# Optimization experiments

Measured on AMD Instinct MI355X. Metric: run time of the kernel, lower is better.

## Reference

```python
import jax, jax.numpy as jnp
import numpy as np

B, Q, C, N_PER, GS = 8, 2048, 256, 64, 8
H1, H2 = 256, 64
EPS = 1e-5


def make_grid():
    a = jnp.linspace(-0.1, 0.1, GS)
    gx, gy = jnp.meshgrid(a, a, indexing='ij')  # torch.meshgrid default 'ij'
    return jnp.stack([gx.reshape(-1), gy.reshape(-1)], axis=1)  # (n, 2)


def setup_inputs() -> dict:
    key = jax.random.key(0)
    ks = jax.random.split(key, 10)
    s = lambda k, shp, fan: jax.random.normal(k, shp, jnp.float32) / np.sqrt(fan)
    return {
        'tokens': jax.random.normal(ks[0], (B, Q, C), jnp.float32),
        'grid': make_grid(),
        'Wc': s(ks[1], (C, 3), C), 'bc': jnp.zeros((3,), jnp.float32),
        'W1': s(ks[2], (C + 2, H1), C + 2), 'b1': jnp.zeros((H1,), jnp.float32),
        'gamma1': jnp.ones((H1,), jnp.float32), 'beta1': jnp.zeros((H1,), jnp.float32),
        'W2': s(ks[3], (H1, H2), H1), 'b2': jnp.zeros((H2,), jnp.float32),
        'gamma2': jnp.ones((H2,), jnp.float32), 'beta2': jnp.zeros((H2,), jnp.float32),
        'W3': s(ks[4], (H2, 3), H2), 'b3': jnp.zeros((3,), jnp.float32),
    }


def batchnorm(x, gamma, beta):
    # BatchNorm1d in training mode: stats over batch (B*Q) and length (n) dims,
    # per channel (last axis here).
    mean = jnp.mean(x, axis=(0, 1, 2), keepdims=True)
    var = jnp.var(x, axis=(0, 1, 2), keepdims=True)
    return gamma * (x - mean) * jax.lax.rsqrt(var + EPS) + beta


def reference(tokens, grid, Wc, bc, W1, b1, gamma1, beta1, W2, b2, gamma2, beta2, W3, b3):
    coarse = tokens @ Wc + bc  # (B, Q, 3)
    # conv1 (1x1) on concat([tokens_expanded, grid]) == split matmul + broadcast add;
    # avoids materializing the (B,Q,n,C+2) concat explicitly.
    tok_part = tokens @ W1[:C]                 # (B, Q, H1)
    grid_part = grid @ W1[C:]                  # (n, H1)
    h = tok_part[:, :, None, :] + grid_part[None, None, :, :] + b1  # (B, Q, n, H1)
    h = jax.nn.relu(batchnorm(h, gamma1, beta1))
    h = jnp.einsum('bqnc,cd->bqnd', h, W2) + b2  # (B, Q, n, H2)
    h = jax.nn.relu(batchnorm(h, gamma2, beta2))
    disp = jnp.einsum('bqnc,cd->bqnd', h, W3) + b3  # (B, Q, n, 3)
    fine = (coarse[:, :, None, :] + disp).reshape(B, Q * N_PER, 3)
    return coarse, fine
```

## Files before the change

### kernel.cpp

```cpp
#include <hip/hip_runtime.h>
#include <hip/hip_bf16.h>

#define ROWS 16384
#define C_   256
#define H1_  256
#define H2_  64
#define EPSN 1e-5f

typedef __bf16 bf16x8 __attribute__((ext_vector_type(8)));
typedef __bf16 bf16x4 __attribute__((ext_vector_type(4)));
typedef __bf16 bf16x2 __attribute__((ext_vector_type(2)));
typedef float  f32x4  __attribute__((ext_vector_type(4)));
typedef float  f32x2  __attribute__((ext_vector_type(2)));

__device__ __forceinline__ bf16x2 cvt2(float a, float b) {
#if __has_builtin(__builtin_amdgcn_cvt_pk_bf16_f32)
    return __builtin_bit_cast(bf16x2, __builtin_amdgcn_cvt_pk_bf16_f32(a, b));
#else
    bf16x2 r; r[0] = (__bf16)a; r[1] = (__bf16)b; return r;
#endif
}

__device__ __forceinline__ void barrier_lgkm() {
    asm volatile("s_waitcnt lgkmcnt(0)" ::: "memory");
    __builtin_amdgcn_sched_barrier(0);
    __builtin_amdgcn_s_barrier();
    __builtin_amdgcn_sched_barrier(0);
}

__global__ __launch_bounds__(256) void k0_pack(const float* __restrict__ W1,
                                               const float* __restrict__ W2,
                                               const float* __restrict__ W3,
                                               __bf16* __restrict__ W1p,
                                               __bf16* __restrict__ W2p,
                                               __bf16* __restrict__ W3p,
                                               float* __restrict__ zero_base) {
    int idx = blockIdx.x * 256 + threadIdx.x;
    if (idx < 65536) {
        int j = idx & 7, l = (idx >> 3) & 63, rest = idx >> 9;
        int ks = rest & 7, CT = rest >> 3;
        int k = ks * 32 + ((l >> 4) << 3) + j;
        int c = CT * 16 + (l & 15);
        W1p[idx] = (__bf16)W1[k * H1_ + c];
    } else {
        int i2 = idx - 65536;
        int j = i2 & 7, l = (i2 >> 3) & 63, rest = i2 >> 9;
        int ks = rest & 7, CK = rest >> 3;
        int k = ks * 32 + ((l >> 4) << 3) + j;
        int c2 = CK * 16 + (l & 15);
        W2p[i2] = (__bf16)W2[k * H2_ + c2];
    }
    if (idx < 1024) {
        int j = idx & 7, l = (idx >> 3) & 63, ks = idx >> 9;
        int k = ks * 32 + ((l >> 4) << 3) + j;
        int c = l & 15;
        W3p[idx] = (c < 3) ? (__bf16)W3[k * 3 + c] : (__bf16)0.f;
    }
    if (idx < 24576) zero_base[idx] = 0.0f;
}

__device__ __forceinline__ void prep_ctx(const float* __restrict__ grid,
                                         const float* __restrict__ W1,
                                         const float* __restrict__ a1p, int c0,
                                         f32x2* wgx2, f32x2* wgy2, float* A_) {
#pragma unroll
    for (int j = 0; j < 8; ++j) A_[j] = grid[2 * j + 1];
    f32x4 a0 = *(const f32x4*)(a1p + c0), a1h = *(const f32x4*)(a1p + c0 + 4);
    f32x4 x0 = *(const f32x4*)(W1 + C_ * H1_ + c0), x1 = *(const f32x4*)(W1 + C_ * H1_ + c0 + 4);
    f32x4 y0 = *(const f32x4*)(W1 + (C_ + 1) * H1_ + c0), yh = *(const f32x4*)(W1 + (C_ + 1) * H1_ + c0 + 4);
    float av[8] = {a0[0], a0[1], a0[2], a0[3], a1h[0], a1h[1], a1h[2], a1h[3]};
    float wx[8] = {x0[0], x0[1], x0[2], x0[3], x1[0], x1[1], x1[2], x1[3]};
    float wy[8] = {y0[0], y0[1], y0[2], y0[3], yh[0], yh[1], yh[2], yh[3]};
#pragma unroll
    for (int e = 0; e < 4; ++e) {
        wgx2[e][0] = av[2 * e] * wx[2 * e];     wgx2[e][1] = av[2 * e + 1] * wx[2 * e + 1];
        wgy2[e][0] = av[2 * e] * wy[2 * e];     wgy2[e][1] = av[2 * e + 1] * wy[2 * e + 1];
    }
}

__device__ __forceinline__ void stage16(__bf16* __restrict__ y1, int w, int c0, int nh,
                                        const float* __restrict__ a1p,
                                        const float* __restrict__ d1p,
                                        const f32x2* wgx2, const f32x2* wgy2,
                                        const float* A_, f32x4 t0, f32x4 t1) {
    f32x4 a0 = *(const f32x4*)(a1p + c0), a1h = *(const f32x4*)(a1p + c0 + 4);
    f32x4 d0 = *(const f32x4*)(d1p + c0), d1h = *(const f32x4*)(d1p + c0 + 4);
    int chunk = c0 >> 3;
    f32x2 base2[4];
    base2[0][0] = fmaf(a0[0], t0[0], d0[0]);  base2[0][1] = fmaf(a0[1], t0[1], d0[1]);
    base2[1][0] = fmaf(a0[2], t0[2], d0[2]);  base2[1][1] = fmaf(a0[3], t0[3], d0[3]);
    base2[2][0] = fmaf(a1h[0], t1[0], d1h[0]); base2[2][1] = fmaf(a1h[1], t1[1], d1h[1]);
    base2[3][0] = fmaf(a1h[2], t1[2], d1h[2]); base2[3][1] = fmaf(a1h[3], t1[3], d1h[3]);
#pragma unroll
    for (int ih = 0; ih < 2; ++ih) {
        float axs = A_[2 * w + ih];
        f32x2 ax2 = {axs, axs};
        f32x2 tc2[4];
#pragma unroll
        for (int e = 0; e < 4; ++e) tc2[e] = __builtin_elementwise_fma(wgx2[e], ax2, base2[e]);
#pragma unroll
        for (int kk = 0; kk < 4; ++kk) {
            int iy = nh + 2 * kk;
            float ays = A_[iy];
            f32x2 ay2 = {ays, ays};
            f32x2 z = {0.f, 0.f};
            int n = w * 16 + ih * 8 + iy;
            bf16x8 out;
            bf16x2* o2 = (bf16x2*)&out;
#pragma unroll
            for (int e = 0; e < 4; ++e) {
                f32x2 v = __builtin_elementwise_max(
                    __builtin_elementwise_fma(wgy2[e], ay2, tc2[e]), z);
                o2[e] = cvt2(v[0], v[1]);
            }
            *(bf16x8*)(&y1[n * 256 + ((chunk ^ iy) << 3)]) = out;
        }
    }
}

__global__ __launch_bounds__(256) void k1a(const float* __restrict__ tokens,
                                           const __bf16* __restrict__ W1p,
                                           const float* __restrict__ Wc,
                                           const float* __restrict__ bc,
                                           float* __restrict__ tokpart,
                                           float* __restrict__ coarse,
                                           float* __restrict__ p1s,
                                           float* __restrict__ p1q) {
    __shared__ __align__(16) __bf16 Al[16 * 264];
    int t = threadIdx.x, w = t >> 6, l = t & 63;
    int quad = l >> 4, col = l & 15;
    int rowbase = (blockIdx.x >> 1) * 16;
    int colhalf = blockIdx.x & 1;
    int slot = blockIdx.x & 31;

    bf16x8 bfr[16];
#pragma unroll
    for (int ctl = 0; ctl < 2; ++ctl)
#pragma unroll
        for (int ks = 0; ks < 8; ++ks) {
            int CT = colhalf * 8 + w * 2 + ctl;
            bfr[ctl * 8 + ks] = *(const bf16x8*)(W1p + (((CT * 8 + ks) * 64 + l) * 8));
        }
    {
        int r = t >> 4, cb = (t & 15) * 16;
        const float* src = tokens + (size_t)(rowbase + r) * C_ + cb;
        f32x4 t0 = *(const f32x4*)(src);
        f32x4 t1 = *(const f32x4*)(src + 4);
        f32x4 t2 = *(const f32x4*)(src + 8);
        f32x4 t3 = *(const f32x4*)(src + 12);
        bf16x8 v0, v1;
        bf16x2* p0 = (bf16x2*)&v0; bf16x2* p1 = (bf16x2*)&v1;
        p0[0] = cvt2(t0[0], t0[1]); p0[1] = cvt2(t0[2], t0[3]);
        p0[2] = cvt2(t1[0], t1[1]); p0[3] = cvt2(t1[2], t1[3]);
        p1[0] = cvt2(t2[0], t2[1]); p1[1] = cvt2(t2[2], t2[3]);
        p1[2] = cvt2(t3[0], t3[1]); p1[3] = cvt2(t3[2], t3[3]);
        *(bf16x8*)(&Al[r * 264 + cb]) = v0;
        *(bf16x8*)(&Al[r * 264 + cb + 8]) = v1;
    }
    barrier_lgkm();

    bf16x8 af[8];
#pragma unroll
    for (int ks = 0; ks < 8; ++ks)
        af[ks] = *(const bf16x8*)(&Al[col * 264 + ks * 32 + quad * 8]);

#pragma unroll
    for (int ctl = 0; ctl < 2; ++ctl) {
        f32x4 acc = {0.f, 0.f, 0.f, 0.f};
#pragma unroll
        for (int ks = 0; ks < 8; ++ks)
            acc = __builtin_amdgcn_mfma_f32_16x16x32_bf16(af[ks], bfr[ctl * 8 + ks], acc, 0, 0, 0);
        int c = colhalf * 128 + w * 32 + ctl * 16 + col;
        float s = 0.f, q = 0.f;
#pragma unroll
        for (int rr = 0; rr < 4; ++rr) {
            float v = acc[rr];
            tokpart[(size_t)(rowbase + quad * 4 + rr) * C_ + c] = v;
            s += v; q += v * v;
        }
        s += __shfl_xor(s, 16, 64); s += __shfl_xor(s, 32, 64);
        q += __shfl_xor(q, 16, 64); q += __shfl_xor(q, 32, 64);
        if (l < 16) {
            int cc = colhalf * 128 + w * 32 + ctl * 16 + l;
            atomicAdd(p1s + slot * C_ + cc, s);
            atomicAdd(p1q + slot * C_ + cc, q);
        }
    }
    if (colhalf == 0) {
        const f32x4* wcp = (const f32x4*)(Wc + l * 12);
        f32x4 wa = wcp[0], wb = wcp[1], wv = wcp[2];
        float wcl[12] = {wa[0], wa[1], wa[2], wa[3], wb[0], wb[1], wb[2], wb[3],
                         wv[0], wv[1], wv[2], wv[3]};
#pragma unroll
        for (int rr = 0; rr < 4; ++rr) {
            int r = w * 4 + rr;
            bf16x4 tv4 = *(const bf16x4*)(&Al[r * 264 + l * 4]);
            float p[3] = {0.f, 0.f, 0.f};
#pragma unroll
            for (int i = 0; i < 4; ++i) {
                float tvf = (float)tv4[i];
#pragma unroll
                for (int j = 0; j < 3; ++j) p[j] = fmaf(tvf, wcl[i * 3 + j], p[j]);
            }
#pragma unroll
            for (int off = 1; off < 64; off <<= 1)
#pragma unroll
                for (int j = 0; j < 3; ++j) p[j] += __shfl_xor(p[j], off, 64);
            if (l == 0) {
#pragma unroll
                for (int j = 0; j < 3; ++j)
                    coarse[(size_t)(rowbase + r) * 3 + j] = p[j] + bc[j];
            }
        }
    }
}

__global__ void k1b(const float* __restrict__ grid, const float* __restrict__ W1,
                    const float* __restrict__ gamma1, const float* __restrict__ beta1,
                    const float* __restrict__ p1s, const float* __restrict__ p1q,
                    float* __restrict__ a1o, float* __restrict__ d1o) {
    int t = threadIdx.x;
    float S = 0.f, Qq = 0.f;
    for (int s = 0; s < 32; ++s) { S += p1s[s * C_ + t]; Qq += p1q[s * C_ + t]; }
    float mean_t = S / (float)ROWS;
    float var_t = Qq / (float)ROWS - mean_t * mean_t;
    float wx = W1[C_ * H1_ + t];
    float wy = W1[(C_ + 1) * H1_ + t];
    float mg = 0.f, qg = 0.f;
    for (int n = 0; n < 64; ++n) {
        float gv = grid[2 * n] * wx + grid[2 * n + 1] * wy;
        mg += gv; qg += gv * gv;
    }
    mg *= (1.f / 64.f);
    float var_g = qg * (1.f / 64.f) - mg * mg;
    float a1 = gamma1[t] * rsqrtf(var_t + var_g + EPSN);
    a1o[t] = a1;
    d1o[t] = beta1[t] - a1 * (mean_t + mg);
}

template <bool SPILL>
__global__ __launch_bounds__(256) void k2(const float* __restrict__ tokpart,
                                          const float* __restrict__ grid,
                                          const float* __restrict__ W1,
                                          const __bf16* __restrict__ W2p,
                                          const float* __restrict__ a1,
                                          const float* __restrict__ d1,
                                          float* __restrict__ p2s,
                                          float* __restrict__ p2q,
                                          __bf16* __restrict__ h2s) {
    __shared__ __align__(16) __bf16 y1[64 * 256];
    int t = threadIdx.x, w = t >> 6, l = t & 63;
    int quad = l >> 4, col = l & 15;
    int wn = w >> 1, wc = w & 1;
    int c0 = (l & 31) * 8, nh = l >> 5;
    int sw = col & 7;

    bf16x8 bfr[16];
#pragma unroll
    for (int ck = 0; ck < 2; ++ck)
#pragma unroll
        for (int ks = 0; ks < 8; ++ks)
            bfr[ck * 8 + ks] = *(const bf16x8*)(W2p + ((((wc * 2 + ck) * 8 + ks) * 64 + l) * 8));

    f32x2 wgx2[4], wgy2[4]; float A_[8];
    prep_ctx(grid, W1, a1, c0, wgx2, wgy2, A_);

    float s[2][4] = {}, q[2][4] = {};

    const float* tokbase = tokpart + (size_t)blockIdx.x * 8 * C_;
    f32x4 t0 = *(const f32x4*)(tokbase + c0);
    f32x4 t1 = *(const f32x4*)(tokbase + c0 + 4);

#pragma unroll 1
    for (int r8 = 0; r8 < 8; ++r8) {
        int row = blockIdx.x * 8 + r8;
        int nr = (r8 < 7) ? (r8 + 1) : 7;
        f32x4 n0 = *(const f32x4*)(tokbase + (size_t)nr * C_ + c0);
        f32x4 n1 = *(const f32x4*)(tokbase + (size_t)nr * C_ + c0 + 4);

        stage16(y1, w, c0, nh, a1, d1, wgx2, wgy2, A_, t0, t1);
        barrier_lgkm();
#pragma unroll
        for (int rt = 0; rt < 2; ++rt) {
            int rowb = (wn * 32 + rt * 16 + col) * 256;
            bf16x8 af[8];
#pragma unroll
            for (int ks = 0; ks < 8; ++ks)
                af[ks] = *(const bf16x8*)(&y1[rowb + (((ks * 4 + quad) ^ sw) << 3)]);
#pragma unroll
            for (int ck = 0; ck < 2; ++ck) {
                f32x4 acc = {0.f, 0.f, 0.f, 0.f};
#pragma unroll
                for (int ks = 0; ks < 8; ++ks)
                    acc = __builtin_amdgcn_mfma_f32_16x16x32_bf16(bfr[ck * 8 + ks], af[ks], acc, 0, 0, 0);
#pragma unroll
                for (int rr = 0; rr < 4; ++rr) {
                    s[ck][rr] += acc[rr];
                    q[ck][rr] += acc[rr] * acc[rr];
                }
                if constexpr (SPILL) {
                    bf16x4 v; bf16x2* v2 = (bf16x2*)&v;
                    v2[0] = cvt2(acc[0], acc[1]);
                    v2[1] = cvt2(acc[2], acc[3]);
                    *(bf16x4*)(h2s + (size_t)row * 4096 +
                               ((wn * 2 + rt) * 4 + wc * 2 + ck) * 256 + l * 4) = v;
                }
            }
        }
        barrier_lgkm();
        t0 = n0; t1 = n1;
    }
    int slot = ((blockIdx.x << 1) | wn) & 63;
#pragma unroll
    for (int ck = 0; ck < 2; ++ck)
#pragma unroll
        for (int rr = 0; rr < 4; ++rr) {
            float sv = s[ck][rr], qv = q[ck][rr];
            sv += __shfl_xor(sv, 1, 64); sv += __shfl_xor(sv, 2, 64);
            sv += __shfl_xor(sv, 4, 64); sv += __shfl_xor(sv, 8, 64);
            qv += __shfl_xor(qv, 1, 64); qv += __shfl_xor(qv, 2, 64);
            qv += __shfl_xor(qv, 4, 64); qv += __shfl_xor(qv, 8, 64);
            if (col == 0) {
                int c2 = wc * 32 + ck * 16 + quad * 4 + rr;
                atomicAdd(p2s + slot * H2_ + c2, sv);
                atomicAdd(p2q + slot * H2_ + c2, qv);
            }
        }
}

__global__ void k2b(const float* __restrict__ p2s, const float* __restrict__ p2q,
                    const float* __restrict__ gamma2, const float* __restrict__ beta2,
                    float* __restrict__ a2o, float* __restrict__ d2o) {
    int t = threadIdx.x;
    float S = 0.f, Qq = 0.f;
    for (int s = 0; s < 64; ++s) { S += p2s[s * H2_ + t]; Qq += p2q[s * H2_ + t]; }
    const float invN = 1.f / ((float)ROWS * 64.f);
    float mean = S * invN;
    float var = Qq * invN - mean * mean;
    float a2 = gamma2[t] * rsqrtf(var + EPSN);
    a2o[t] = a2;
    d2o[t] = beta2[t] - a2 * mean;
}

__global__ __launch_bounds__(256) void k3s(const __bf16* __restrict__ h2s,
                                           const float* __restrict__ a2,
                                           const float* __restrict__ d2p,
                                           const __bf16* __restrict__ W3p,
                                           const float* __restrict__ b3,
                                           const float* __restrict__ coarse,
                                           float* __restrict__ fine) {
    __shared__ __align__(16) __bf16 y2l[4][16 * 64];
    __shared__ __align__(16) float finebuf[8 * 192];
    int t = threadIdx.x, w = t >> 6, l = t & 63;
    int quad = l >> 4, col = l & 15;
    int sw = col & 7;

    bf16x8 wfr[2];
#pragma unroll
    for (int ks = 0; ks < 2; ++ks)
        wfr[ks] = *(const bf16x8*)(W3p + ((ks * 64 + l) * 8));

    float a2v[16], d2v[16];
#pragma unroll
    for (int ck = 0; ck < 4; ++ck)
#pragma unroll
        for (int rr = 0; rr < 4; ++rr) {
            int c2 = ck * 16 + quad * 4 + rr;
            a2v[ck * 4 + rr] = a2[c2];
            d2v[ck * 4 + rr] = d2p[c2];
        }
    float b3v = (col < 3) ? b3[col] : 0.f;
    __bf16* yw = &y2l[w][0];

#pragma unroll 1
    for (int r8 = 0; r8 < 8; ++r8) {
        int row = blockIdx.x * 8 + r8;
        const __bf16* src = h2s + (size_t)row * 4096 + l * 4;
        bf16x4 u[4];
#pragma unroll
        for (int ck = 0; ck < 4; ++ck)
            u[ck] = *(const bf16x4*)(src + (w * 4 + ck) * 256);
#pragma unroll
        for (int ck = 0; ck < 4; ++ck) {
            float y0 = fmaxf(fmaf(a2v[ck * 4 + 0], (float)u[ck][0], d2v[ck * 4 + 0]), 0.f);
            float y1v = fmaxf(fmaf(a2v[ck * 4 + 1], (float)u[ck][1], d2v[ck * 4 + 1]), 0.f);
            float y2 = fmaxf(fmaf(a2v[ck * 4 + 2], (float)u[ck][2], d2v[ck * 4 + 2]), 0.f);
            float y3 = fmaxf(fmaf(a2v[ck * 4 + 3], (float)u[ck][3], d2v[ck * 4 + 3]), 0.f);
            bf16x4 v; bf16x2* v2 = (bf16x2*)&v;
            v2[0] = cvt2(y0, y1v); v2[1] = cvt2(y2, y3);
            int chunk = ck * 2 + (quad >> 1);
            *(bf16x4*)(&yw[col * 64 + ((chunk ^ sw) << 3) + (quad & 1) * 4]) = v;
        }
        bf16x8 af2[2];
#pragma unroll
        for (int ks = 0; ks < 2; ++ks)
            af2[ks] = *(const bf16x8*)(&yw[col * 64 + (((ks * 4 + quad) ^ sw) << 3)]);
        f32x4 acc = {0.f, 0.f, 0.f, 0.f};
        acc = __builtin_amdgcn_mfma_f32_16x16x32_bf16(af2[0], wfr[0], acc, 0, 0, 0);
        acc = __builtin_amdgcn_mfma_f32_16x16x32_bf16(af2[1], wfr[1], acc, 0, 0, 0);
        if (col < 3) {
            float cj = coarse[row * 3 + col] + b3v;
#pragma unroll
            for (int rr = 0; rr < 4; ++rr)
                finebuf[r8 * 192 + (w * 16 + quad * 4 + rr) * 3 + col] = acc[rr] + cj;
        }
    }
    __syncthreads();
    {
        float* dst = fine + (size_t)blockIdx.x * 1536;
        const f32x4* fb = (const f32x4*)finebuf;
        *(f32x4*)(dst + 4 * t) = fb[t];
        if (t < 128) *(f32x4*)(dst + 1024 + 4 * t) = fb[256 + t];
    }
}

__global__ __launch_bounds__(256) void k3r(const float* __restrict__ tokpart,
                                           const float* __restrict__ grid,
                                           const float* __restrict__ W1,
                                           const __bf16* __restrict__ W2p,
                                           const float* __restrict__ a1,
                                           const float* __restrict__ d1,
                                           const __bf16* __restrict__ W3p,
                                           const float* __restrict__ a2,
                                           const float* __restrict__ d2p,
                                           const float* __restrict__ b3,
                                           const float* __restrict__ coarse,
                                           float* __restrict__ fine) {
    __shared__ __align__(16) __bf16 y1[64 * 256];
    __shared__ __align__(16) __bf16 y2l[64 * 72];
    __shared__ __align__(16) float finebuf[8 * 192];
    int t = threadIdx.x, w = t >> 6, l = t & 63;
    int quad = l >> 4, col = l & 15;
    int wn = w >> 1, wc = w & 1;
    int c0 = (l & 31) * 8, nh = l >> 5;
    int sw = col & 7;

    bf16x8 bfr[16];
#pragma unroll
    for (int ck = 0; ck < 2; ++ck)
#pragma unroll
        for (int ks = 0; ks < 8; ++ks)
            bfr[ck * 8 + ks] = *(const bf16x8*)(W2p + ((((wc * 2 + ck) * 8 + ks) * 64 + l) * 8));
    bf16x8 wfr[2];
#pragma unroll
    for (int ks = 0; ks < 2; ++ks)
        wfr[ks] = *(const bf16x8*)(W3p + ((ks * 64 + l) * 8));

    f32x2 wgx2[4], wgy2[4]; float A_[8];
    prep_ctx(grid, W1, a1, c0, wgx2, wgy2, A_);

    float a2v[8], d2v[8];
#pragma unroll
    for (int ck = 0; ck < 2; ++ck)
#pragma unroll
        for (int rr = 0; rr < 4; ++rr) {
            int c2 = wc * 32 + ck * 16 + quad * 4 + rr;
            a2v[ck * 4 + rr] = a2[c2];
            d2v[ck * 4 + rr] = d2p[c2];
        }
    float b3v = (col < 3) ? b3[col] : 0.f;

#pragma unroll 1
    for (int r8 = 0; r8 < 8; ++r8) {
        int row = blockIdx.x * 8 + r8;
        const float* tokrow = tokpart + (size_t)row * C_;
        f32x4 t0 = *(const f32x4*)(tokrow + c0);
        f32x4 t1 = *(const f32x4*)(tokrow + c0 + 4);
        stage16(y1, w, c0, nh, a1, d1, wgx2, wgy2, A_, t0, t1);
        __syncthreads();
#pragma unroll
        for (int rt = 0; rt < 2; ++rt) {
            int rowb = (wn * 32 + rt * 16 + col) * 256;
            bf16x8 af[8];
#pragma unroll
            for (int ks = 0; ks < 8; ++ks)
                af[ks] = *(const bf16x8*)(&y1[rowb + (((ks * 4 + quad) ^ sw) << 3)]);
#pragma unroll
            for (int ck = 0; ck < 2; ++ck) {
                f32x4 acc = {0.f, 0.f, 0.f, 0.f};
#pragma unroll
                for (int ks = 0; ks < 8; ++ks)
                    acc = __builtin_amdgcn_mfma_f32_16x16x32_bf16(bfr[ck * 8 + ks], af[ks], acc, 0, 0, 0);
                bf16x4 v; bf16x2* v2 = (bf16x2*)&v;
                float y0 = fmaxf(fmaf(a2v[ck * 4 + 0], acc[0], d2v[ck * 4 + 0]), 0.f);
                float y1v = fmaxf(fmaf(a2v[ck * 4 + 1], acc[1], d2v[ck * 4 + 1]), 0.f);
                float y2 = fmaxf(fmaf(a2v[ck * 4 + 2], acc[2], d2v[ck * 4 + 2]), 0.f);
                float y3 = fmaxf(fmaf(a2v[ck * 4 + 3], acc[3], d2v[ck * 4 + 3]), 0.f);
                v2[0] = cvt2(y0, y1v); v2[1] = cvt2(y2, y3);
                *(bf16x4*)(&y2l[(wn * 32 + rt * 16 + col) * 72 + wc * 32 + ck * 16 + quad * 4]) = v;
            }
        }
        __syncthreads();
        bf16x8 af2[2];
#pragma unroll
        for (int ks = 0; ks < 2; ++ks)
            af2[ks] = *(const bf16x8*)(&y2l[(w * 16 + col) * 72 + ks * 32 + quad * 8]);
        f32x4 d2acc = {0.f, 0.f, 0.f, 0.f};
        d2acc = __builtin_amdgcn_mfma_f32_16x16x32_bf16(af2[0], wfr[0], d2acc, 0, 0, 0);
        d2acc = __builtin_amdgcn_mfma_f32_16x16x32_bf16(af2[1], wfr[1], d2acc, 0, 0, 0);
        if (col < 3) {
            float cj = coarse[row * 3 + col] + b3v;
#pragma unroll
            for (int rr = 0; rr < 4; ++rr)
                finebuf[r8 * 192 + (w * 16 + quad * 4 + rr) * 3 + col] = d2acc[rr] + cj;
        }
        __syncthreads();
    }
    {
        float* dst = fine + (size_t)blockIdx.x * 1536;
        const f32x4* fb = (const f32x4*)finebuf;
        *(f32x4*)(dst + 4 * t) = fb[t];
        if (t < 128) *(f32x4*)(dst + 1024 + 4 * t) = fb[256 + t];
    }
}

extern "C" void kernel_launch(void* const* d_in, const int* in_sizes, int n_in,
                              void* d_out, int out_size, void* d_ws, size_t ws_size,
                              hipStream_t stream) {
    (void)in_sizes; (void)n_in; (void)out_size;
    const float* tokens = (const float*)d_in[0];
    const float* grid   = (const float*)d_in[1];
    const float* Wc     = (const float*)d_in[2];
    const float* bc     = (const float*)d_in[3];
    const float* W1     = (const float*)d_in[4];
    const float* gamma1 = (const float*)d_in[6];
    const float* beta1  = (const float*)d_in[7];
    const float* W2     = (const float*)d_in[8];
    const float* gamma2 = (const float*)d_in[10];
    const float* beta2  = (const float*)d_in[11];
    const float* W3     = (const float*)d_in[12];
    const float* b3     = (const float*)d_in[13];

    char* ws = (char*)d_ws;
    __bf16* W1p     = (__bf16*)(ws);
    __bf16* W2p     = (__bf16*)(ws + 131072);
    float*  p1s     = (float*)(ws + 163840);
    float*  p1q     = (float*)(ws + 196608);
    float*  p2s     = (float*)(ws + 229376);
    float*  p2q     = (float*)(ws + 245760);
    float*  a1      = (float*)(ws + 262144);
    float*  d1      = (float*)(ws + 263168);
    float*  a2      = (float*)(ws + 264192);
    float*  d2p     = (float*)(ws + 264448);
    __bf16* W3p     = (__bf16*)(ws + 264704);
    float*  tokpart = (float*)(ws + 266752);
    __bf16* h2s     = (__bf16*)(ws + 17043968);

    const size_t SPILL_NEED = 17043968ull + 134217728ull;
    bool spill = ws_size >= SPILL_NEED;

    float* coarse = (float*)d_out;
    float* fine   = (float*)d_out + (size_t)ROWS * 3;

    k0_pack<<<320, 256, 0, stream>>>(W1, W2, W3, W1p, W2p, W3p, p1s);
    k1a<<<2048, 256, 0, stream>>>(tokens, W1p, Wc, bc, tokpart, coarse, p1s, p1q);
    k1b<<<1, 256, 0, stream>>>(grid, W1, gamma1, beta1, p1s, p1q, a1, d1);
    if (spill) {
        k2<true><<<ROWS / 8, 256, 0, stream>>>(tokpart, grid, W1, W2p, a1, d1, p2s, p2q, h2s);
        k2b<<<1, 64, 0, stream>>>(p2s, p2q, gamma2, beta2, a2, d2p);
        k3s<<<ROWS / 8, 256, 0, stream>>>(h2s, a2, d2p, W3p, b3, coarse, fine);
    } else {
        k2<false><<<ROWS / 8, 256, 0, stream>>>(tokpart, grid, W1, W2p, a1, d1, p2s, p2q, h2s);
        k2b<<<1, 64, 0, stream>>>(p2s, p2q, gamma2, beta2, a2, d2p);
        k3r<<<ROWS / 8, 256, 0, stream>>>(tokpart, grid, W1, W2p, a1, d1, W3p, a2, d2p, b3, coarse, fine);
    }
}
```

Baseline: 194.7 us.

## Fold BatchNorm stat finalization into consumer kernels, drop single-block launches

Removes the two single-block kernels that turned partial sums into BatchNorm scale/shift (k1b, k2b). Each block of k2, k3s and k3r now reduces the partial sums itself into shared memory at startup. The grid-dependent mean and variance terms move into block 0 of the pack kernel. This removes two serialized tiny launches and their pipeline bubbles, at the cost of every block redundantly reading the 32x256 or 64x64 partial-sum arrays and doing the reduction.

```diff
diff --git a/kernel.cpp b/kernel.cpp
--- a/kernel.cpp
+++ b/kernel.cpp
@@ -31,10 +31,14 @@
 __global__ __launch_bounds__(256) void k0_pack(const float* __restrict__ W1,
                                                const float* __restrict__ W2,
                                                const float* __restrict__ W3,
+                                               const float* __restrict__ grid,
                                                __bf16* __restrict__ W1p,
                                                __bf16* __restrict__ W2p,
                                                __bf16* __restrict__ W3p,
-                                               float* __restrict__ zero_base) {
+                                               float* __restrict__ zero_base,
+                                               float* __restrict__ gm,
+                                               float* __restrict__ gvv) {
+    __shared__ float gl[128];
     int idx = blockIdx.x * 256 + threadIdx.x;
     if (idx < 65536) {
         int j = idx & 7, l = (idx >> 3) & 63, rest = idx >> 9;
@@ -57,11 +61,27 @@
         W3p[idx] = (c < 3) ? (__bf16)W3[k * 3 + c] : (__bf16)0.f;
     }
     if (idx < 24576) zero_base[idx] = 0.0f;
+    if (blockIdx.x == 0) {
+        int t = threadIdx.x;
+        if (t < 128) gl[t] = grid[t];
+        __syncthreads();
+        float wx = W1[C_ * H1_ + t];
+        float wy = W1[(C_ + 1) * H1_ + t];
+        float mg = 0.f, qg = 0.f;
+#pragma unroll
+        for (int n = 0; n < 64; ++n) {
+            float gv = gl[2 * n] * wx + gl[2 * n + 1] * wy;
+            mg += gv; qg = fmaf(gv, gv, qg);
+        }
+        mg *= (1.f / 64.f);
+        gm[t] = mg;
+        gvv[t] = qg * (1.f / 64.f) - mg * mg;
+    }
 }
 
 __device__ __forceinline__ void prep_ctx(const float* __restrict__ grid,
                                          const float* __restrict__ W1,
-                                         const float* __restrict__ a1p, int c0,
+                                         const float* a1p, int c0,
                                          f32x2* wgx2, f32x2* wgy2, float* A_) {
 #pragma unroll
     for (int j = 0; j < 8; ++j) A_[j] = grid[2 * j + 1];
@@ -79,8 +99,8 @@
 }
 
 __device__ __forceinline__ void stage16(__bf16* __restrict__ y1, int w, int c0, int nh,
-                                        const float* __restrict__ a1p,
-                                        const float* __restrict__ d1p,
+                                        const float* a1p,
+                                        const float* d1p,
                                         const f32x2* wgx2, const f32x2* wgy2,
                                         const float* A_, f32x4 t0, f32x4 t1) {
     f32x4 a0 = *(const f32x4*)(a1p + c0), a1h = *(const f32x4*)(a1p + c0 + 4);
@@ -115,6 +135,47 @@
             }
             *(bf16x8*)(&y1[n * 256 + ((chunk ^ iy) << 3)]) = out;
         }
+    }
+}
+
+__device__ __forceinline__ void bn1_fold(const float* __restrict__ p1s,
+                                         const float* __restrict__ p1q,
+                                         const float* __restrict__ gamma1,
+                                         const float* __restrict__ beta1,
+                                         const float* __restrict__ gm,
+                                         const float* __restrict__ gvv,
+                                         float* a1l, float* d1l, int t) {
+    float S = 0.f, Q = 0.f;
+#pragma unroll 8
+    for (int s2 = 0; s2 < 32; ++s2) {
+        S += p1s[s2 * C_ + t];
+        Q += p1q[s2 * C_ + t];
+    }
+    float mean_t = S / (float)ROWS;
+    float var_t = Q / (float)ROWS - mean_t * mean_t;
+    float a1v = gamma1[t] * rsqrtf(var_t + gvv[t] + EPSN);
+    a1l[t] = a1v;
+    d1l[t] = beta1[t] - a1v * (mean_t + gm[t]);
+}
+
+__device__ __forceinline__ void bn2_fold(const float* __restrict__ p2s,
+                                         const float* __restrict__ p2q,
+                                         const float* __restrict__ gamma2,
+                                         const float* __restrict__ beta2,
+                                         float* a2l, float* d2l, int t) {
+    if (t < H2_) {
+        float S = 0.f, Q = 0.f;
+#pragma unroll 8
+        for (int s2 = 0; s2 < 64; ++s2) {
+            S += p2s[s2 * H2_ + t];
+            Q += p2q[s2 * H2_ + t];
+        }
+        const float invN = 1.f / ((float)ROWS * 64.f);
+        float mean = S * invN;
+        float var = Q * invN - mean * mean;
+        float a2v = gamma2[t] * rsqrtf(var + EPSN);
+        a2l[t] = a2v;
+        d2l[t] = beta2[t] - a2v * mean;
     }
 }
 
@@ -215,46 +276,30 @@
     }
 }
 
-__global__ void k1b(const float* __restrict__ grid, const float* __restrict__ W1,
-                    const float* __restrict__ gamma1, const float* __restrict__ beta1,
-                    const float* __restrict__ p1s, const float* __restrict__ p1q,
-                    float* __restrict__ a1o, float* __restrict__ d1o) {
-    int t = threadIdx.x;
-    float S = 0.f, Qq = 0.f;
-    for (int s = 0; s < 32; ++s) { S += p1s[s * C_ + t]; Qq += p1q[s * C_ + t]; }
-    float mean_t = S / (float)ROWS;
-    float var_t = Qq / (float)ROWS - mean_t * mean_t;
-    float wx = W1[C_ * H1_ + t];
-    float wy = W1[(C_ + 1) * H1_ + t];
-    float mg = 0.f, qg = 0.f;
-    for (int n = 0; n < 64; ++n) {
-        float gv = grid[2 * n] * wx + grid[2 * n + 1] * wy;
-        mg += gv; qg += gv * gv;
-    }
-    mg *= (1.f / 64.f);
-    float var_g = qg * (1.f / 64.f) - mg * mg;
-    float a1 = gamma1[t] * rsqrtf(var_t + var_g + EPSN);
-    a1o[t] = a1;
-    d1o[t] = beta1[t] - a1 * (mean_t + mg);
-}
-
 template <bool SPILL>
 __global__ __launch_bounds__(256) void k2(const float* __restrict__ tokpart,
                                           const float* __restrict__ grid,
                                           const float* __restrict__ W1,
                                           const __bf16* __restrict__ W2p,
-                                          const float* __restrict__ a1,
-                                          const float* __restrict__ d1,
+                                          const float* __restrict__ p1s,
+                                          const float* __restrict__ p1q,
+                                          const float* __restrict__ gamma1,
+                                          const float* __restrict__ beta1,
+                                          const float* __restrict__ gm,
+                                          const float* __restrict__ gvv,
                                           float* __restrict__ p2s,
                                           float* __restrict__ p2q,
                                           __bf16* __restrict__ h2s) {
     __shared__ __align__(16) __bf16 y1[64 * 256];
+    __shared__ __align__(16) float a1l[256], d1l[256];
     int t = threadIdx.x, w = t >> 6, l = t & 63;
     int quad = l >> 4, col = l & 15;
     int wn = w >> 1, wc = w & 1;
     int c0 = (l & 31) * 8, nh = l >> 5;
     int sw = col & 7;
 
+    bn1_fold(p1s, p1q, gamma1, beta1, gm, gvv, a1l, d1l, t);
+
     bf16x8 bfr[16];
 #pragma unroll
     for (int ck = 0; ck < 2; ++ck)
@@ -262,8 +307,10 @@
         for (int ks = 0; ks < 8; ++ks)
             bfr[ck * 8 + ks] = *(const bf16x8*)(W2p + ((((wc * 2 + ck) * 8 + ks) * 64 + l) * 8));
 
+    barrier_lgkm();
+
     f32x2 wgx2[4], wgy2[4]; float A_[8];
-    prep_ctx(grid, W1, a1, c0, wgx2, wgy2, A_);
+    prep_ctx(grid, W1, a1l, c0, wgx2, wgy2, A_);
 
     float s[2][4] = {}, q[2][4] = {};
 
@@ -278,7 +325,7 @@
         f32x4 n0 = *(const f32x4*)(tokbase + (size_t)nr * C_ + c0);
         f32x4 n1 = *(const f32x4*)(tokbase + (size_t)nr * C_ + c0 + 4);
 
-        stage16(y1, w, c0, nh, a1, d1, wgx2, wgy2, A_, t0, t1);
+        stage16(y1, w, c0, nh, a1l, d1l, wgx2, wgy2, A_, t0, t1);
         barrier_lgkm();
 #pragma unroll
         for (int rt = 0; rt < 2; ++rt) {
@@ -328,46 +375,39 @@
         }
 }
 
-__global__ void k2b(const float* __restrict__ p2s, const float* __restrict__ p2q,
-                    const float* __restrict__ gamma2, const float* __restrict__ beta2,
-                    float* __restrict__ a2o, float* __restrict__ d2o) {
-    int t = threadIdx.x;
-    float S = 0.f, Qq = 0.f;
-    for (int s = 0; s < 64; ++s) { S += p2s[s * H2_ + t]; Qq += p2q[s * H2_ + t]; }
-    const float invN = 1.f / ((float)ROWS * 64.f);
-    float mean = S * invN;
-    float var = Qq * invN - mean * mean;
-    float a2 = gamma2[t] * rsqrtf(var + EPSN);
-    a2o[t] = a2;
-    d2o[t] = beta2[t] - a2 * mean;
-}
-
 __global__ __launch_bounds__(256) void k3s(const __bf16* __restrict__ h2s,
-                                           const float* __restrict__ a2,
-                                           const float* __restrict__ d2p,
+                                           const float* __restrict__ p2s,
+                                           const float* __restrict__ p2q,
+                                           const float* __restrict__ gamma2,
+                                           const float* __restrict__ beta2,
                                            const __bf16* __restrict__ W3p,
                                            const float* __restrict__ b3,
                                            const float* __restrict__ coarse,
                                            float* __restrict__ fine) {
     __shared__ __align__(16) __bf16 y2l[4][16 * 64];
     __shared__ __align__(16) float finebuf[8 * 192];
+    __shared__ __align__(16) float a2l[64], d2l[64];
     int t = threadIdx.x, w = t >> 6, l = t & 63;
     int quad = l >> 4, col = l & 15;
     int sw = col & 7;
 
+    bn2_fold(p2s, p2q, gamma2, beta2, a2l, d2l, t);
+
     bf16x8 wfr[2];
 #pragma unroll
     for (int ks = 0; ks < 2; ++ks)
         wfr[ks] = *(const bf16x8*)(W3p + ((ks * 64 + l) * 8));
 
+    barrier_lgkm();
+
     float a2v[16], d2v[16];
 #pragma unroll
     for (int ck = 0; ck < 4; ++ck)
 #pragma unroll
         for (int rr = 0; rr < 4; ++rr) {
             int c2 = ck * 16 + quad * 4 + rr;
-            a2v[ck * 4 + rr] = a2[c2];
-            d2v[ck * 4 + rr] = d2p[c2];
+            a2v[ck * 4 + rr] = a2l[c2];
+            d2v[ck * 4 + rr] = d2l[c2];
         }
     float b3v = (col < 3) ? b3[col] : 0.f;
     __bf16* yw = &y2l[w][0];
@@ -418,23 +458,34 @@
                                            const float* __restrict__ grid,
                                            const float* __restrict__ W1,
                                            const __bf16* __restrict__ W2p,
-                                           const float* __restrict__ a1,
-                                           const float* __restrict__ d1,
+                                           const float* __restrict__ p1s,
+                                           const float* __restrict__ p1q,
+                                           const float* __restrict__ gamma1,
+                                           const float* __restrict__ beta1,
+                                           const float* __restrict__ gm,
+                                           const float* __restrict__ gvv,
                                            const __bf16* __restrict__ W3p,
-                                           const float* __restrict__ a2,
-                                           const float* __restrict__ d2p,
+                                           const float* __restrict__ p2s,
+                                           const float* __restrict__ p2q,
+                                           const float* __restrict__ gamma2,
+                                           const float* __restrict__ beta2,
                                            const float* __restrict__ b3,
                                            const float* __restrict__ coarse,
                                            float* __restrict__ fine) {
     __shared__ __align__(16) __bf16 y1[64 * 256];
     __shared__ __align__(16) __bf16 y2l[64 * 72];
     __shared__ __align__(16) float finebuf[8 * 192];
+    __shared__ __align__(16) float a1l[256], d1l[256];
+    __shared__ __align__(16) float a2l[64], d2l[64];
     int t = threadIdx.x, w = t >> 6, l = t & 63;
     int quad = l >> 4, col = l & 15;
     int wn = w >> 1, wc = w & 1;
     int c0 = (l & 31) * 8, nh = l >> 5;
     int sw = col & 7;
 
+    bn1_fold(p1s, p1q, gamma1, beta1, gm, gvv, a1l, d1l, t);
+    bn2_fold(p2s, p2q, gamma2, beta2, a2l, d2l, t);
+
     bf16x8 bfr[16];
 #pragma unroll
     for (int ck = 0; ck < 2; ++ck)
@@ -446,8 +497,10 @@
     for (int ks = 0; ks < 2; ++ks)
         wfr[ks] = *(const bf16x8*)(W3p + ((ks * 64 + l) * 8));
 
+    barrier_lgkm();
+
     f32x2 wgx2[4], wgy2[4]; float A_[8];
-    prep_ctx(grid, W1, a1, c0, wgx2, wgy2, A_);
+    prep_ctx(grid, W1, a1l, c0, wgx2, wgy2, A_);
 
     float a2v[8], d2v[8];
 #pragma unroll
@@ -455,8 +508,8 @@
 #pragma unroll
         for (int rr = 0; rr < 4; ++rr) {
             int c2 = wc * 32 + ck * 16 + quad * 4 + rr;
-            a2v[ck * 4 + rr] = a2[c2];
-            d2v[ck * 4 + rr] = d2p[c2];
+            a2v[ck * 4 + rr] = a2l[c2];
+            d2v[ck * 4 + rr] = d2l[c2];
         }
     float b3v = (col < 3) ? b3[col] : 0.f;
 
@@ -466,7 +519,7 @@
         const float* tokrow = tokpart + (size_t)row * C_;
         f32x4 t0 = *(const f32x4*)(tokrow + c0);
         f32x4 t1 = *(const f32x4*)(tokrow + c0 + 4);
-        stage16(y1, w, c0, nh, a1, d1, wgx2, wgy2, A_, t0, t1);
+        stage16(y1, w, c0, nh, a1l, d1l, wgx2, wgy2, A_, t0, t1);
         __syncthreads();
 #pragma unroll
         for (int rt = 0; rt < 2; ++rt) {
@@ -538,10 +591,8 @@
     float*  p1q     = (float*)(ws + 196608);
     float*  p2s     = (float*)(ws + 229376);
     float*  p2q     = (float*)(ws + 245760);
-    float*  a1      = (float*)(ws + 262144);
-    float*  d1      = (float*)(ws + 263168);
-    float*  a2      = (float*)(ws + 264192);
-    float*  d2p     = (float*)(ws + 264448);
+    float*  gm      = (float*)(ws + 262144);
+    float*  gvv     = (float*)(ws + 263168);
     __bf16* W3p     = (__bf16*)(ws + 264704);
     float*  tokpart = (float*)(ws + 266752);
     __bf16* h2s     = (__bf16*)(ws + 17043968);
@@ -552,16 +603,18 @@
     float* coarse = (float*)d_out;
     float* fine   = (float*)d_out + (size_t)ROWS * 3;
 
-    k0_pack<<<320, 256, 0, stream>>>(W1, W2, W3, W1p, W2p, W3p, p1s);
+    k0_pack<<<320, 256, 0, stream>>>(W1, W2, W3, grid, W1p, W2p, W3p, p1s, gm, gvv);
     k1a<<<2048, 256, 0, stream>>>(tokens, W1p, Wc, bc, tokpart, coarse, p1s, p1q);
-    k1b<<<1, 256, 0, stream>>>(grid, W1, gamma1, beta1, p1s, p1q, a1, d1);
     if (spill) {
-        k2<true><<<ROWS / 8, 256, 0, stream>>>(tokpart, grid, W1, W2p, a1, d1, p2s, p2q, h2s);
-        k2b<<<1, 64, 0, stream>>>(p2s, p2q, gamma2, beta2, a2, d2p);
-        k3s<<<ROWS / 8, 256, 0, stream>>>(h2s, a2, d2p, W3p, b3, coarse, fine);
+        k2<true><<<ROWS / 8, 256, 0, stream>>>(tokpart, grid, W1, W2p, p1s, p1q,
+                                               gamma1, beta1, gm, gvv, p2s, p2q, h2s);
+        k3s<<<ROWS / 8, 256, 0, stream>>>(h2s, p2s, p2q, gamma2, beta2, W3p, b3,
+                                          coarse, fine);
     } else {
-        k2<false><<<ROWS / 8, 256, 0, stream>>>(tokpart, grid, W1, W2p, a1, d1, p2s, p2q, h2s);
-        k2b<<<1, 64, 0, stream>>>(p2s, p2q, gamma2, beta2, a2, d2p);
-        k3r<<<ROWS / 8, 256, 0, stream>>>(tokpart, grid, W1, W2p, a1, d1, W3p, a2, d2p, b3, coarse, fine);
-    }
-}
+        k2<false><<<ROWS / 8, 256, 0, stream>>>(tokpart, grid, W1, W2p, p1s, p1q,
+                                                gamma1, beta1, gm, gvv, p2s, p2q, h2s);
+        k3r<<<ROWS / 8, 256, 0, stream>>>(tokpart, grid, W1, W2p, p1s, p1q,
+                                          gamma1, beta1, gm, gvv, W3p, p2s, p2q,
+                                          gamma2, beta2, b3, coarse, fine);
+    }
+}
```

New measurement: 202.7 us. +4.1%, slower.

## Drop h2 spill path, always recompute in k3r with prefetched token rows

Applied to the files above, without the earlier changes.

Removes the optional path that wrote the 128 MB bf16 layer-2 activation buffer in k2 and read it back in k3s. The final kernel now always recomputes layer 1 and layer 2 from tokpart. k3r also gains next-row token prefetch and lighter LDS-only barriers, and the grid-statistics loop moves from the single-block k1b into k0_pack. The aim is to trade heavy HBM write and read traffic for extra MFMA recompute and to shorten the serial k1b kernel. The recompute doubles the layer-1/layer-2 GEMM work.

```diff
diff --git a/kernel.cpp b/kernel.cpp
--- a/kernel.cpp
+++ b/kernel.cpp
@@ -31,10 +31,14 @@
 __global__ __launch_bounds__(256) void k0_pack(const float* __restrict__ W1,
                                                const float* __restrict__ W2,
                                                const float* __restrict__ W3,
+                                               const float* __restrict__ grid,
                                                __bf16* __restrict__ W1p,
                                                __bf16* __restrict__ W2p,
                                                __bf16* __restrict__ W3p,
-                                               float* __restrict__ zero_base) {
+                                               float* __restrict__ zero_base,
+                                               float* __restrict__ gm,
+                                               float* __restrict__ gvv) {
+    __shared__ float gl[128];
     int idx = blockIdx.x * 256 + threadIdx.x;
     if (idx < 65536) {
         int j = idx & 7, l = (idx >> 3) & 63, rest = idx >> 9;
@@ -57,6 +61,22 @@
         W3p[idx] = (c < 3) ? (__bf16)W3[k * 3 + c] : (__bf16)0.f;
     }
     if (idx < 24576) zero_base[idx] = 0.0f;
+    if (blockIdx.x == 0) {
+        int t = threadIdx.x;
+        if (t < 128) gl[t] = grid[t];
+        __syncthreads();
+        float wx = W1[C_ * H1_ + t];
+        float wy = W1[(C_ + 1) * H1_ + t];
+        float mg = 0.f, qg = 0.f;
+#pragma unroll
+        for (int n = 0; n < 64; ++n) {
+            float gv = gl[2 * n] * wx + gl[2 * n + 1] * wy;
+            mg += gv; qg = fmaf(gv, gv, qg);
+        }
+        mg *= (1.f / 64.f);
+        gm[t] = mg;
+        gvv[t] = qg * (1.f / 64.f) - mg * mg;
+    }
 }
 
 __device__ __forceinline__ void prep_ctx(const float* __restrict__ grid,
@@ -215,30 +235,21 @@
     }
 }
 
-__global__ void k1b(const float* __restrict__ grid, const float* __restrict__ W1,
+__global__ void k1b(const float* __restrict__ gm, const float* __restrict__ gvv,
                     const float* __restrict__ gamma1, const float* __restrict__ beta1,
                     const float* __restrict__ p1s, const float* __restrict__ p1q,
                     float* __restrict__ a1o, float* __restrict__ d1o) {
     int t = threadIdx.x;
-    float S = 0.f, Qq = 0.f;
-    for (int s = 0; s < 32; ++s) { S += p1s[s * C_ + t]; Qq += p1q[s * C_ + t]; }
+    float S = 0.f, Q = 0.f;
+#pragma unroll 8
+    for (int s = 0; s < 32; ++s) { S += p1s[s * C_ + t]; Q += p1q[s * C_ + t]; }
     float mean_t = S / (float)ROWS;
-    float var_t = Qq / (float)ROWS - mean_t * mean_t;
-    float wx = W1[C_ * H1_ + t];
-    float wy = W1[(C_ + 1) * H1_ + t];
-    float mg = 0.f, qg = 0.f;
-    for (int n = 0; n < 64; ++n) {
-        float gv = grid[2 * n] * wx + grid[2 * n + 1] * wy;
-        mg += gv; qg += gv * gv;
-    }
-    mg *= (1.f / 64.f);
-    float var_g = qg * (1.f / 64.f) - mg * mg;
-    float a1 = gamma1[t] * rsqrtf(var_t + var_g + EPSN);
+    float var_t = Q / (float)ROWS - mean_t * mean_t;
+    float a1 = gamma1[t] * rsqrtf(var_t + gvv[t] + EPSN);
     a1o[t] = a1;
-    d1o[t] = beta1[t] - a1 * (mean_t + mg);
-}
-
-template <bool SPILL>
+    d1o[t] = beta1[t] - a1 * (mean_t + gm[t]);
+}
+
 __global__ __launch_bounds__(256) void k2(const float* __restrict__ tokpart,
                                           const float* __restrict__ grid,
                                           const float* __restrict__ W1,
@@ -246,8 +257,7 @@
                                           const float* __restrict__ a1,
                                           const float* __restrict__ d1,
                                           float* __restrict__ p2s,
-                                          float* __restrict__ p2q,
-                                          __bf16* __restrict__ h2s) {
+                                          float* __restrict__ p2q) {
     __shared__ __align__(16) __bf16 y1[64 * 256];
     int t = threadIdx.x, w = t >> 6, l = t & 63;
     int quad = l >> 4, col = l & 15;
@@ -273,7 +283,6 @@
 
 #pragma unroll 1
     for (int r8 = 0; r8 < 8; ++r8) {
-        int row = blockIdx.x * 8 + r8;
         int nr = (r8 < 7) ? (r8 + 1) : 7;
         f32x4 n0 = *(const f32x4*)(tokbase + (size_t)nr * C_ + c0);
         f32x4 n1 = *(const f32x4*)(tokbase + (size_t)nr * C_ + c0 + 4);
@@ -297,13 +306,6 @@
                 for (int rr = 0; rr < 4; ++rr) {
                     s[ck][rr] += acc[rr];
                     q[ck][rr] += acc[rr] * acc[rr];
-                }
-                if constexpr (SPILL) {
-                    bf16x4 v; bf16x2* v2 = (bf16x2*)&v;
-                    v2[0] = cvt2(acc[0], acc[1]);
-                    v2[1] = cvt2(acc[2], acc[3]);
-                    *(bf16x4*)(h2s + (size_t)row * 4096 +
-                               ((wn * 2 + rt) * 4 + wc * 2 + ck) * 256 + l * 4) = v;
                 }
             }
         }
@@ -332,86 +334,15 @@
                     const float* __restrict__ gamma2, const float* __restrict__ beta2,
                     float* __restrict__ a2o, float* __restrict__ d2o) {
     int t = threadIdx.x;
-    float S = 0.f, Qq = 0.f;
-    for (int s = 0; s < 64; ++s) { S += p2s[s * H2_ + t]; Qq += p2q[s * H2_ + t]; }
+    float S = 0.f, Q = 0.f;
+#pragma unroll 8
+    for (int s = 0; s < 64; ++s) { S += p2s[s * H2_ + t]; Q += p2q[s * H2_ + t]; }
     const float invN = 1.f / ((float)ROWS * 64.f);
     float mean = S * invN;
-    float var = Qq * invN - mean * mean;
+    float var = Q * invN - mean * mean;
     float a2 = gamma2[t] * rsqrtf(var + EPSN);
     a2o[t] = a2;
     d2o[t] = beta2[t] - a2 * mean;
-}
-
-__global__ __launch_bounds__(256) void k3s(const __bf16* __restrict__ h2s,
-                                           const float* __restrict__ a2,
-                                           const float* __restrict__ d2p,
-                                           const __bf16* __restrict__ W3p,
-                                           const float* __restrict__ b3,
-                                           const float* __restrict__ coarse,
-                                           float* __restrict__ fine) {
-    __shared__ __align__(16) __bf16 y2l[4][16 * 64];
-    __shared__ __align__(16) float finebuf[8 * 192];
-    int t = threadIdx.x, w = t >> 6, l = t & 63;
-    int quad = l >> 4, col = l & 15;
-    int sw = col & 7;
-
-    bf16x8 wfr[2];
-#pragma unroll
-    for (int ks = 0; ks < 2; ++ks)
-        wfr[ks] = *(const bf16x8*)(W3p + ((ks * 64 + l) * 8));
-
-    float a2v[16], d2v[16];
-#pragma unroll
-    for (int ck = 0; ck < 4; ++ck)
-#pragma unroll
-        for (int rr = 0; rr < 4; ++rr) {
-            int c2 = ck * 16 + quad * 4 + rr;
-            a2v[ck * 4 + rr] = a2[c2];
-            d2v[ck * 4 + rr] = d2p[c2];
-        }
-    float b3v = (col < 3) ? b3[col] : 0.f;
-    __bf16* yw = &y2l[w][0];
-
-#pragma unroll 1
-    for (int r8 = 0; r8 < 8; ++r8) {
-        int row = blockIdx.x * 8 + r8;
-        const __bf16* src = h2s + (size_t)row * 4096 + l * 4;
-        bf16x4 u[4];
-#pragma unroll
-        for (int ck = 0; ck < 4; ++ck)
-            u[ck] = *(const bf16x4*)(src + (w * 4 + ck) * 256);
-#pragma unroll
-        for (int ck = 0; ck < 4; ++ck) {
-            float y0 = fmaxf(fmaf(a2v[ck * 4 + 0], (float)u[ck][0], d2v[ck * 4 + 0]), 0.f);
-            float y1v = fmaxf(fmaf(a2v[ck * 4 + 1], (float)u[ck][1], d2v[ck * 4 + 1]), 0.f);
-            float y2 = fmaxf(fmaf(a2v[ck * 4 + 2], (float)u[ck][2], d2v[ck * 4 + 2]), 0.f);
-            float y3 = fmaxf(fmaf(a2v[ck * 4 + 3], (float)u[ck][3], d2v[ck * 4 + 3]), 0.f);
-            bf16x4 v; bf16x2* v2 = (bf16x2*)&v;
-            v2[0] = cvt2(y0, y1v); v2[1] = cvt2(y2, y3);
-            int chunk = ck * 2 + (quad >> 1);
-            *(bf16x4*)(&yw[col * 64 + ((chunk ^ sw) << 3) + (quad & 1) * 4]) = v;
-        }
-        bf16x8 af2[2];
-#pragma unroll
-        for (int ks = 0; ks < 2; ++ks)
-            af2[ks] = *(const bf16x8*)(&yw[col * 64 + (((ks * 4 + quad) ^ sw) << 3)]);
-        f32x4 acc = {0.f, 0.f, 0.f, 0.f};
-        acc = __builtin_amdgcn_mfma_f32_16x16x32_bf16(af2[0], wfr[0], acc, 0, 0, 0);
-        acc = __builtin_amdgcn_mfma_f32_16x16x32_bf16(af2[1], wfr[1], acc, 0, 0, 0);
-        if (col < 3) {
-            float cj = coarse[row * 3 + col] + b3v;
-#pragma unroll
-            for (int rr = 0; rr < 4; ++rr)
-                finebuf[r8 * 192 + (w * 16 + quad * 4 + rr) * 3 + col] = acc[rr] + cj;
-        }
-    }
-    __syncthreads();
-    {
-        float* dst = fine + (size_t)blockIdx.x * 1536;
-        const f32x4* fb = (const f32x4*)finebuf;
-        *(f32x4*)(dst + 4 * t) = fb[t];
-        if (t < 128) *(f32x4*)(dst + 1024 + 4 * t) = fb[256 + t];
-    }
 }
 
 __global__ __launch_bounds__(256) void k3r(const float* __restrict__ tokpart,
@@ -460,14 +391,19 @@
         }
     float b3v = (col < 3) ? b3[col] : 0.f;
 
+    const float* tokbase = tokpart + (size_t)blockIdx.x * 8 * C_;
+    f32x4 t0 = *(const f32x4*)(tokbase + c0);
+    f32x4 t1 = *(const f32x4*)(tokbase + c0 + 4);
+
 #pragma unroll 1
     for (int r8 = 0; r8 < 8; ++r8) {
         int row = blockIdx.x * 8 + r8;
-        const float* tokrow = tokpart + (size_t)row * C_;
-        f32x4 t0 = *(const f32x4*)(tokrow + c0);
-        f32x4 t1 = *(const f32x4*)(tokrow + c0 + 4);
+        int nr = (r8 < 7) ? (r8 + 1) : 7;
+        f32x4 n0 = *(const f32x4*)(tokbase + (size_t)nr * C_ + c0);
+        f32x4 n1 = *(const f32x4*)(tokbase + (size_t)nr * C_ + c0 + 4);
+
         stage16(y1, w, c0, nh, a1, d1, wgx2, wgy2, A_, t0, t1);
-        __syncthreads();
+        barrier_lgkm();
 #pragma unroll
         for (int rt = 0; rt < 2; ++rt) {
             int rowb = (wn * 32 + rt * 16 + col) * 256;
@@ -490,7 +426,7 @@
                 *(bf16x4*)(&y2l[(wn * 32 + rt * 16 + col) * 72 + wc * 32 + ck * 16 + quad * 4]) = v;
             }
         }
-        __syncthreads();
+        barrier_lgkm();
         bf16x8 af2[2];
 #pragma unroll
         for (int ks = 0; ks < 2; ++ks)
@@ -504,7 +440,8 @@
             for (int rr = 0; rr < 4; ++rr)
                 finebuf[r8 * 192 + (w * 16 + quad * 4 + rr) * 3 + col] = d2acc[rr] + cj;
         }
-        __syncthreads();
+        barrier_lgkm();
+        t0 = n0; t1 = n1;
     }
     {
         float* dst = fine + (size_t)blockIdx.x * 1536;
@@ -517,7 +454,7 @@
 extern "C" void kernel_launch(void* const* d_in, const int* in_sizes, int n_in,
                               void* d_out, int out_size, void* d_ws, size_t ws_size,
                               hipStream_t stream) {
-    (void)in_sizes; (void)n_in; (void)out_size;
+    (void)in_sizes; (void)n_in; (void)out_size; (void)ws_size;
     const float* tokens = (const float*)d_in[0];
     const float* grid   = (const float*)d_in[1];
     const float* Wc     = (const float*)d_in[2];
@@ -543,25 +480,18 @@
     float*  a2      = (float*)(ws + 264192);
     float*  d2p     = (float*)(ws + 264448);
     __bf16* W3p     = (__bf16*)(ws + 264704);
-    float*  tokpart = (float*)(ws + 266752);
-    __bf16* h2s     = (__bf16*)(ws + 17043968);
-
-    const size_t SPILL_NEED = 17043968ull + 134217728ull;
-    bool spill = ws_size >= SPILL_NEED;
+    float*  gm      = (float*)(ws + 266752);
+    float*  gvv     = (float*)(ws + 267776);
+    float*  tokpart = (float*)(ws + 268800);
 
     float* coarse = (float*)d_out;
     float* fine   = (float*)d_out + (size_t)ROWS * 3;
 
-    k0_pack<<<320, 256, 0, stream>>>(W1, W2, W3, W1p, W2p, W3p, p1s);
+    k0_pack<<<320, 256, 0, stream>>>(W1, W2, W3, grid, W1p, W2p, W3p, p1s, gm, gvv);
     k1a<<<2048, 256, 0, stream>>>(tokens, W1p, Wc, bc, tokpart, coarse, p1s, p1q);
-    k1b<<<1, 256, 0, stream>>>(grid, W1, gamma1, beta1, p1s, p1q, a1, d1);
-    if (spill) {
-        k2<true><<<ROWS / 8, 256, 0, stream>>>(tokpart, grid, W1, W2p, a1, d1, p2s, p2q, h2s);
-        k2b<<<1, 64, 0, stream>>>(p2s, p2q, gamma2, beta2, a2, d2p);
-        k3s<<<ROWS / 8, 256, 0, stream>>>(h2s, a2, d2p, W3p, b3, coarse, fine);
-    } else {
-        k2<false><<<ROWS / 8, 256, 0, stream>>>(tokpart, grid, W1, W2p, a1, d1, p2s, p2q, h2s);
-        k2b<<<1, 64, 0, stream>>>(p2s, p2q, gamma2, beta2, a2, d2p);
-        k3r<<<ROWS / 8, 256, 0, stream>>>(tokpart, grid, W1, W2p, a1, d1, W3p, a2, d2p, b3, coarse, fine);
-    }
-}
+    k1b<<<1, 256, 0, stream>>>(gm, gvv, gamma1, beta1, p1s, p1q, a1, d1);
+    k2<<<ROWS / 8, 256, 0, stream>>>(tokpart, grid, W1, W2p, a1, d1, p2s, p2q);
+    k2b<<<1, 64, 0, stream>>>(p2s, p2q, gamma2, beta2, a2, d2p);
+    k3r<<<ROWS / 8, 256, 0, stream>>>(tokpart, grid, W1, W2p, a1, d1,
+                                      W3p, a2, d2p, b3, coarse, fine);
+}
```

Result: slower. 227.4 us (+16.8%).
